# Kernel tuning notes

Hardware: AMD Instinct MI355X
Metric: run time of the kernel (lower is better)

Reference implementation:

```python
import jax, jax.numpy as jnp
import numpy as np

B, M = 32768, 200
NUM_LAYERS, OW, OH = 22, 11, 11
CNN_CH, HIDDEN = 128, 512
ACTION_NVEC = (9, 10)


def setup_inputs() -> dict:
    key = jax.random.key(0)
    ks = jax.random.split(key, 16)
    s = 0.02
    inp = {
        "observations": jax.random.randint(ks[0], (B, M, 3), 0, 256, dtype=jnp.int32),
        "max_vec": jnp.ones((NUM_LAYERS,), dtype=jnp.float32),
        "w_conv1": jax.random.normal(ks[1], (CNN_CH, NUM_LAYERS, 5, 5), jnp.float32) * s,
        "b_conv1": jnp.zeros((CNN_CH,), jnp.float32),
        "w_conv2": jax.random.normal(ks[2], (CNN_CH, CNN_CH, 3, 3), jnp.float32) * s,
        "b_conv2": jnp.zeros((CNN_CH,), jnp.float32),
        "w_fc": jax.random.normal(ks[3], (CNN_CH, HIDDEN // 2), jnp.float32) * s,
        "b_fc": jnp.zeros((HIDDEN // 2,), jnp.float32),
        "w_self": jax.random.normal(ks[4], (NUM_LAYERS, HIDDEN // 2), jnp.float32) * s,
        "b_self": jnp.zeros((HIDDEN // 2,), jnp.float32),
        "w_actor0": jax.random.normal(ks[5], (HIDDEN, ACTION_NVEC[0]), jnp.float32) * 0.01,
        "b_actor0": jnp.zeros((ACTION_NVEC[0],), jnp.float32),
        "w_actor1": jax.random.normal(ks[6], (HIDDEN, ACTION_NVEC[1]), jnp.float32) * 0.01,
        "b_actor1": jnp.zeros((ACTION_NVEC[1],), jnp.float32),
        "w_value": jax.random.normal(ks[7], (HIDDEN, 1), jnp.float32) * s,
        "b_value": jnp.zeros((1,), jnp.float32),
    }
    return inp


def _conv(x, w, b, stride):
    y = jax.lax.conv_general_dilated(
        x, w, window_strides=(stride, stride), padding="VALID",
        dimension_numbers=("NCHW", "OIHW", "NCHW"))
    return y + b[None, :, None, None]


def _encode(observations, max_vec, w_conv1, b_conv1, w_conv2, b_conv2,
            w_fc, b_fc, w_self, b_self):
    # torch: token_observations[token_observations == 255] = 0
    obs = jnp.where(observations == 255, 0, observations)
    coords = obs[..., 0]                       # [B, M]
    x_idx = (coords >> 4) & 15
    y_idx = coords & 15
    atr_idx = obs[..., 1]
    atr_val = obs[..., 2].astype(jnp.float32)
    # coords_byte != 255 is always True after the 255->0 rewrite above
    valid = (x_idx < OW) & (y_idx < OH) & (atr_idx < NUM_LAYERS)
    b_idx = jnp.broadcast_to(jnp.arange(obs.shape[0])[:, None], coords.shape)
    # route invalid tokens to a dummy batch slot B, then drop it
    b_idx = jnp.where(valid, b_idx, obs.shape[0])
    a_idx = jnp.where(valid, atr_idx, 0)
    xs = jnp.where(valid, x_idx, 0)
    ys = jnp.where(valid, y_idx, 0)
    box = jnp.zeros((obs.shape[0] + 1, NUM_LAYERS, OW, OH), jnp.float32)
    box = box.at[b_idx, a_idx, xs, ys].set(atr_val)[: obs.shape[0]]
    features = box / max_vec[None, :, None, None]
    self_feat = jax.nn.relu(features[:, :, 5, 5] @ w_self + b_self)   # [B, 256]
    h = jax.nn.relu(_conv(features, w_conv1, b_conv1, 3))             # [B,128,3,3]
    h = jax.nn.relu(_conv(h, w_conv2, b_conv2, 1))                    # [B,128,1,1]
    h = h.reshape(h.shape[0], -1)                                     # [B,128]
    cnn_feat = jax.nn.relu(h @ w_fc + b_fc)                           # [B,256]
    return jnp.concatenate([self_feat, cnn_feat], axis=1)             # [B,512]


def reference(observations, max_vec, w_conv1, b_conv1, w_conv2, b_conv2,
              w_fc, b_fc, w_self, b_self, w_actor0, b_actor0,
              w_actor1, b_actor1, w_value, b_value):
    hidden = _encode(observations, max_vec, w_conv1, b_conv1, w_conv2, b_conv2,
                     w_fc, b_fc, w_self, b_self)
    logits0 = hidden @ w_actor0 + b_actor0
    logits1 = hidden @ w_actor1 + b_actor1
    value = hidden @ w_value + b_value
    return (logits0, logits1, value, hidden)
```

## Files before the change

kernel.cpp:

```cpp
#include <hip/hip_runtime.h>
#include <hip/hip_bf16.h>

typedef unsigned int uint;
typedef unsigned short ushort;
typedef unsigned long long ull;
typedef __attribute__((ext_vector_type(8))) short short8;
typedef __attribute__((ext_vector_type(4))) float float4_;

#define B_TOT 32768
#define NL    22
#define HID0  ((long)B_TOT * 20)

#define W2F_OFF  0
#define WFCF_OFF 294912
#define WHF_OFF  360448
#define W1T_OFF  393216
#define H1_OFF   674816

__device__ __forceinline__ ushort f2bf(float v) {
  uint x = __float_as_uint(v);
  x += 0x7fffu + ((x >> 16) & 1u);
  return (ushort)(x >> 16);
}

__device__ __forceinline__ uint cvtpk(float lo, float hi) {
  uint r;
  asm volatile("v_cvt_pk_bf16_f32 %0, %1, %2" : "=v"(r) : "v"(lo), "v"(hi));
  return r;
}

extern "C" __global__ __launch_bounds__(256)
void k_prep(const float* __restrict__ wc1, const float* __restrict__ wc2,
            const float* __restrict__ wfc,
            const float* __restrict__ wa0, const float* __restrict__ wa1,
            const float* __restrict__ wv,
            ushort* __restrict__ w2f, ushort* __restrict__ wfcf,
            ushort* __restrict__ whf, float* __restrict__ w1t)
{
  int i = blockIdx.x * 256 + threadIdx.x;
  if (i < 18432) {
    int l = i & 63, cg = (i >> 6) & 7, ks = i >> 9;
    int col = cg * 16 + (l & 15), kb = ks * 32 + (l >> 4) * 8;
    ushort t[8];
    #pragma unroll
    for (int j = 0; j < 8; ++j) t[j] = f2bf(wc2[col * 1152 + kb + j]);
    uint4 o = { (uint)t[0]|((uint)t[1]<<16), (uint)t[2]|((uint)t[3]<<16),
                (uint)t[4]|((uint)t[5]<<16), (uint)t[6]|((uint)t[7]<<16) };
    ((uint4*)w2f)[i] = o;
  } else if (i < 22528) {
    int i2 = i - 18432;
    int l = i2 & 63, cg = (i2 >> 6) & 15, ks = i2 >> 10;
    int col = cg * 16 + (l & 15), kb = ks * 32 + (l >> 4) * 8;
    ushort t[8];
    #pragma unroll
    for (int j = 0; j < 8; ++j) t[j] = f2bf(wfc[(kb + j) * 256 + col]);
    uint4 o = { (uint)t[0]|((uint)t[1]<<16), (uint)t[2]|((uint)t[3]<<16),
                (uint)t[4]|((uint)t[5]<<16), (uint)t[6]|((uint)t[7]<<16) };
    ((uint4*)wfcf)[i2] = o;
  } else if (i < 24576) {
    int i2 = i - 22528;
    int l = i2 & 63, cg = (i2 >> 6) & 1, ks = i2 >> 7;
    int col = cg * 16 + (l & 15), kb = ks * 32 + (l >> 4) * 8;
    ushort t[8];
    #pragma unroll
    for (int j = 0; j < 8; ++j) {
      int k = kb + j;
      float v = (col < 9)  ? wa0[k*9 + col]
              : (col < 19) ? wa1[k*10 + (col - 9)]
              : (col == 19) ? wv[k] : 0.f;
      t[j] = f2bf(v);
    }
    uint4 o = { (uint)t[0]|((uint)t[1]<<16), (uint)t[2]|((uint)t[3]<<16),
                (uint)t[4]|((uint)t[5]<<16), (uint)t[6]|((uint)t[7]<<16) };
    ((uint4*)whf)[i2] = o;
  } else if (i < 24576 + 70400) {
    int j = i - 24576;
    int oc = j & 127, r = j >> 7;
    w1t[j] = wc1[oc * 550 + r];
  }
}

extern "C" __global__ __launch_bounds__(256)
void k_encode(const int* __restrict__ obs, const float* __restrict__ maxvec,
              const float* __restrict__ w1t, const float* __restrict__ bc1,
              const float* __restrict__ wself, const float* __restrict__ bself,
              float* __restrict__ out, ushort* __restrict__ h1g)
{
  __shared__ uint klist[4][64];

  const int tid = threadIdx.x, lane = tid & 63, w = tid >> 6;
  const long b = (long)blockIdx.x * 4 + w;

  float rm_own = (lane < NL) ? (1.0f / maxvec[lane]) : 0.f;

  const uint* ob = (const uint*)obs + b * 600;
  int cnt = 0;
  #pragma unroll
  for (int r = 0; r < 4; ++r) {
    int m = r * 64 + lane;
    bool valid = false; uint pk = 0;
    if (m < 200) {
      uint c = ob[m*3], a = ob[m*3+1], v = ob[m*3+2];
      c = (c == 255u) ? 0u : c;  a = (a == 255u) ? 0u : a;  v = (v == 255u) ? 0u : v;
      uint x = (c >> 4) & 15u, y = c & 15u;
      valid = (x < 11u) && (y < 11u) && (a < NL);
      pk = (a << 16) | (x << 12) | (y << 8) | v;
    }
    ull bal = __ballot(valid);
    if (valid) {
      int pos = cnt + __popcll(bal & ((1ull << lane) - 1ull));
      if (pos < 64) klist[w][pos] = pk;
    }
    cnt += __popcll(bal);
  }
  if (cnt > 64) cnt = 64;

  uint u = (lane < cnt) ? klist[w][lane] : 0xffffffffu;
  uint cell = u >> 8;
  bool alive = (lane < cnt);
  for (int d = 1; d < cnt; ++d) {
    uint oc_ = __shfl_down(cell, d);
    alive = alive && !((lane + d < cnt) && (oc_ == cell));
  }
  ull bal2 = __ballot(alive);
  const int n2 = __popcll(bal2);
  if (alive) klist[w][__popcll(bal2 & ((1ull << lane) - 1ull))] = u;

  float a0[9] = {0,0,0,0,0,0,0,0,0}, a1[9] = {0,0,0,0,0,0,0,0,0};
  float2 sa = {0.f, 0.f}, sb = {0.f, 0.f};
  uint tk = klist[w][0];
  for (int t = 0; t < n2; ++t) {
    uint cur = tk;
    tk = klist[w][(t + 1) & 63];
    int a = cur >> 16, x = (cur >> 12) & 15, y = (cur >> 8) & 15;
    float fv = (float)(cur & 255u) * __shfl(rm_own, a);
    if (x == 5 && y == 5) {
      const float2* ws2 = (const float2*)(wself + a * 256);
      float2 w0 = ws2[lane], w1 = ws2[64 + lane];
      sa.x = fmaf(fv, w0.x, sa.x);  sa.y = fmaf(fv, w0.y, sa.y);
      sb.x = fmaf(fv, w1.x, sb.x);  sb.y = fmaf(fv, w1.y, sb.y);
    }
    #pragma unroll
    for (int ox = 0; ox < 3; ++ox) {
      int kx = x - 3 * ox;
      if ((unsigned)kx > 4u) continue;
      #pragma unroll
      for (int oy = 0; oy < 3; ++oy) {
        int ky = y - 3 * oy;
        if ((unsigned)ky > 4u) continue;
        float2 wv2 = ((const float2*)(w1t + (a*25 + kx*5 + ky) * 128))[lane];
        a0[ox*3+oy] = fmaf(fv, wv2.x, a0[ox*3+oy]);
        a1[ox*3+oy] = fmaf(fv, wv2.y, a1[ox*3+oy]);
      }
    }
  }

  {
    const float2* bs2 = (const float2*)bself;
    float2 b0_ = bs2[lane], b1_ = bs2[64 + lane];
    float2 o0 = { fmaxf(sa.x + b0_.x, 0.f), fmaxf(sa.y + b0_.y, 0.f) };
    float2 o1 = { fmaxf(sb.x + b1_.x, 0.f), fmaxf(sb.y + b1_.y, 0.f) };
    float2* out2 = (float2*)(out + HID0 + b * 512);
    out2[lane] = o0;
    out2[64 + lane] = o1;
  }

  {
    const float2 bc = ((const float2*)bc1)[lane];
    float v0[9], v1[9];
    #pragma unroll
    for (int p = 0; p < 9; ++p) {
      v0[p] = fmaxf(a0[p] + bc.x, 0.f);
      v1[p] = fmaxf(a1[p] + bc.y, 0.f);
    }
    uint wds[9];
    wds[0] = cvtpk(v0[0], v0[1]);
    wds[1] = cvtpk(v0[2], v0[3]);
    wds[2] = cvtpk(v0[4], v0[5]);
    wds[3] = cvtpk(v0[6], v0[7]);
    wds[4] = cvtpk(v0[8], v1[0]);
    wds[5] = cvtpk(v1[1], v1[2]);
    wds[6] = cvtpk(v1[3], v1[4]);
    wds[7] = cvtpk(v1[5], v1[6]);
    wds[8] = cvtpk(v1[7], v1[8]);
    uint* dst = (uint*)h1g + b * 576 + 9 * lane;
    #pragma unroll
    for (int j = 0; j < 9; ++j) dst[j] = wds[j];
  }
}

extern "C" __global__ __launch_bounds__(256)
void k_mlp(const ushort* __restrict__ h1g, const ushort* __restrict__ w2f,
           const float* __restrict__ bc2, const ushort* __restrict__ wfcf,
           const float* __restrict__ bfc, const ushort* __restrict__ whf,
           const float* __restrict__ ba0, const float* __restrict__ ba1,
           const float* __restrict__ bv, float* __restrict__ out)
{
  __shared__ short  Abuf[2][4][64][8];
  __shared__ ushort h2A[16][64][8];

  const int tid = threadIdx.x, lane = tid & 63, w = tid >> 6;
  const int lo = lane & 15, hi = lane >> 4;
  const int bb = blockIdx.x, b0 = bb * 64;

  const short8* w2fv  = (const short8*)w2f;
  const short8* wfcfv = (const short8*)wfcf;
  const uint4*  A4    = (const uint4*)h1g;
  const long    arow  = (long)(b0 + (tid >> 2)) * 144 + (tid & 3);

  float4_ acc[4][2];
  #pragma unroll
  for (int cgi = 0; cgi < 2; ++cgi) {
    float bv_ = bc2[(2*w + cgi)*16 + lo];
    float4_ t = {bv_, bv_, bv_, bv_};
    #pragma unroll
    for (int m = 0; m < 4; ++m) acc[m][cgi] = t;
  }

  uint4 rA = A4[arow];
  for (int t = 0; t < 36; ++t) {
    const int cur = t & 1;
    *(uint4*)&Abuf[cur][tid & 3][tid >> 2][0] = rA;
    if (t + 1 < 36) rA = A4[arow + (t + 1) * 4];
    __syncthreads();
    short8 af[4];
    #pragma unroll
    for (int m = 0; m < 4; ++m)
      af[m] = *(const short8*)&Abuf[cur][hi][m*16 + lo][0];
    #pragma unroll
    for (int cgi = 0; cgi < 2; ++cgi) {
      short8 bf = w2fv[(t*8 + 2*w + cgi)*64 + lane];
      #pragma unroll
      for (int m = 0; m < 4; ++m)
        acc[m][cgi] = __builtin_amdgcn_mfma_f32_16x16x32_bf16(af[m], bf, acc[m][cgi], 0, 0, 0);
    }
  }
  __syncthreads();

  #pragma unroll
  for (int cgi = 0; cgi < 2; ++cgi) {
    int col = (2*w + cgi)*16 + lo;
    #pragma unroll
    for (int m = 0; m < 4; ++m)
      #pragma unroll
      for (int q = 0; q < 4; ++q) {
        int R = m*16 + hi*4 + q;
        h2A[col >> 3][R][col & 7] = f2bf(fmaxf(acc[m][cgi][q], 0.f));
      }
  }
  __syncthreads();

  float4_ acc2[4][4];
  #pragma unroll
  for (int cgi = 0; cgi < 4; ++cgi) {
    float bv_ = bfc[(4*w + cgi)*16 + lo];
    float4_ t = {bv_, bv_, bv_, bv_};
    #pragma unroll
    for (int m = 0; m < 4; ++m) acc2[m][cgi] = t;
  }
  #pragma unroll
  for (int ks = 0; ks < 4; ++ks) {
    short8 af[4];
    #pragma unroll
    for (int m = 0; m < 4; ++m)
      af[m] = *(const short8*)&h2A[ks*4 + hi][m*16 + lo][0];
    #pragma unroll
    for (int cgi = 0; cgi < 4; ++cgi) {
      short8 bf = wfcfv[(ks*16 + 4*w + cgi)*64 + lane];
      #pragma unroll
      for (int m = 0; m < 4; ++m)
        acc2[m][cgi] = __builtin_amdgcn_mfma_f32_16x16x32_bf16(af[m], bf, acc2[m][cgi], 0, 0, 0);
    }
  }

  #pragma unroll
  for (int cgi = 0; cgi < 4; ++cgi) {
    int col = (4*w + cgi)*16 + lo;
    #pragma unroll
    for (int m = 0; m < 4; ++m)
      #pragma unroll
      for (int q = 0; q < 4; ++q) {
        int R = m*16 + hi*4 + q;
        out[HID0 + (long)(b0 + R)*512 + 256 + col] = fmaxf(acc2[m][cgi][q], 0.f);
      }
  }
  __syncthreads();

  const short8* whfv = (const short8*)whf;
  float4_ acc3[2];
  #pragma unroll
  for (int cg = 0; cg < 2; ++cg) {
    int col = cg*16 + lo;
    float bias = (col < 9) ? ba0[col] : (col < 19) ? ba1[col - 9]
               : (col == 19) ? bv[0] : 0.f;
    float4_ t = {bias, bias, bias, bias};
    acc3[cg] = t;
  }

  const float* hrow = out + HID0 + (long)(b0 + w*16 + lo) * 512;
  #pragma unroll
  for (int ks = 0; ks < 16; ++ks) {
    float4_ f0 = *(const float4_*)(hrow + ks*32 + hi*8);
    float4_ f1 = *(const float4_*)(hrow + ks*32 + hi*8 + 4);
    union { short8 s; ushort u[8]; } afu;
    afu.u[0] = f2bf(f0[0]); afu.u[1] = f2bf(f0[1]);
    afu.u[2] = f2bf(f0[2]); afu.u[3] = f2bf(f0[3]);
    afu.u[4] = f2bf(f1[0]); afu.u[5] = f2bf(f1[1]);
    afu.u[6] = f2bf(f1[2]); afu.u[7] = f2bf(f1[3]);
    #pragma unroll
    for (int cg = 0; cg < 2; ++cg) {
      short8 bf = whfv[(ks*2 + cg)*64 + lane];
      acc3[cg] = __builtin_amdgcn_mfma_f32_16x16x32_bf16(afu.s, bf, acc3[cg], 0, 0, 0);
    }
  }

  #pragma unroll
  for (int cg = 0; cg < 2; ++cg) {
    int col = cg*16 + lo;
    #pragma unroll
    for (int q = 0; q < 4; ++q) {
      long R = b0 + w*16 + hi*4 + q;
      float v = acc3[cg][q];
      if (col < 9)        out[R*9 + col] = v;
      else if (col < 19)  out[(long)B_TOT*9 + R*10 + (col - 9)] = v;
      else if (col == 19) out[(long)B_TOT*19 + R] = v;
    }
  }
}

extern "C" void kernel_launch(void* const* d_in, const int* in_sizes, int n_in,
                              void* d_out, int out_size, void* d_ws, size_t ws_size,
                              hipStream_t stream) {
  const int* obs      = (const int*)d_in[0];
  const float* maxvec = (const float*)d_in[1];
  const float* wc1    = (const float*)d_in[2];
  const float* bc1    = (const float*)d_in[3];
  const float* wc2    = (const float*)d_in[4];
  const float* bc2    = (const float*)d_in[5];
  const float* wfc    = (const float*)d_in[6];
  const float* bfc    = (const float*)d_in[7];
  const float* wself  = (const float*)d_in[8];
  const float* bself  = (const float*)d_in[9];
  const float* wa0    = (const float*)d_in[10];
  const float* ba0    = (const float*)d_in[11];
  const float* wa1    = (const float*)d_in[12];
  const float* ba1    = (const float*)d_in[13];
  const float* wv     = (const float*)d_in[14];
  const float* bv     = (const float*)d_in[15];
  float* out          = (float*)d_out;

  char* ws = (char*)d_ws;
  ushort* w2f  = (ushort*)(ws + W2F_OFF);
  ushort* wfcf = (ushort*)(ws + WFCF_OFF);
  ushort* whf  = (ushort*)(ws + WHF_OFF);
  float*  w1t  = (float*)(ws + W1T_OFF);
  ushort* h1g  = (ushort*)(ws + H1_OFF);

  k_prep  <<<dim3(371),      dim3(256), 0, stream>>>(wc1, wc2, wfc, wa0, wa1, wv,
                                                     w2f, wfcf, whf, w1t);
  k_encode<<<dim3(B_TOT/4),  dim3(256), 0, stream>>>(obs, maxvec, w1t, bc1,
                                                     wself, bself, out, h1g);
  k_mlp   <<<dim3(B_TOT/64), dim3(256), 0, stream>>>(h1g, w2f, bc2, wfcf, bfc,
                                                     whf, ba0, ba1, bv, out);
}
```

Baseline: 109.5 us.

## Fuse encoder and MLP kernels, keeping conv1 activations in LDS

Merges the token-scatter/conv1 encoder and the conv2/fc/head MLP into one kernel that processes 32 samples per block. The conv1 output stays in shared memory instead of going through a global workspace, and conv2 weights are re-laid out (channel-major within position) to match. Token broadcast now uses readfirstlane/readlane instead of shuffles. The cost is about 77KB of LDS per block, which lowers occupancy, each wave runs 8 samples serially, and the MFMA tiles shrink to 32 rows.

New measurement: 161.6 us. 1.48x slower.

```diff
diff --git a/kernel.cpp b/kernel.cpp
--- a/kernel.cpp
+++ b/kernel.cpp
@@ -15,14 +15,15 @@
 #define WFCF_OFF 294912
 #define WHF_OFF  360448
 #define W1T_OFF  393216
-#define H1_OFF   674816
+
+#define H1_LDS_BYTES 76032
+#define LDS_TOTAL    77056
 
 __device__ __forceinline__ ushort f2bf(float v) {
   uint x = __float_as_uint(v);
   x += 0x7fffu + ((x >> 16) & 1u);
   return (ushort)(x >> 16);
 }
-
 __device__ __forceinline__ uint cvtpk(float lo, float hi) {
   uint r;
   asm volatile("v_cvt_pk_bf16_f32 %0, %1, %2" : "=v"(r) : "v"(lo), "v"(hi));
@@ -43,7 +44,10 @@
     int col = cg * 16 + (l & 15), kb = ks * 32 + (l >> 4) * 8;
     ushort t[8];
     #pragma unroll
-    for (int j = 0; j < 8; ++j) t[j] = f2bf(wc2[col * 1152 + kb + j]);
+    for (int j = 0; j < 8; ++j) {
+      int kp = kb + j, ic = kp & 127, p = kp >> 7;
+      t[j] = f2bf(wc2[col * 1152 + ic * 9 + p]);
+    }
     uint4 o = { (uint)t[0]|((uint)t[1]<<16), (uint)t[2]|((uint)t[3]<<16),
                 (uint)t[4]|((uint)t[5]<<16), (uint)t[6]|((uint)t[7]<<16) };
     ((uint4*)w2f)[i] = o;
@@ -81,203 +85,175 @@
 }
 
 extern "C" __global__ __launch_bounds__(256)
-void k_encode(const int* __restrict__ obs, const float* __restrict__ maxvec,
-              const float* __restrict__ w1t, const float* __restrict__ bc1,
-              const float* __restrict__ wself, const float* __restrict__ bself,
-              float* __restrict__ out, ushort* __restrict__ h1g)
+void k_main(const int* __restrict__ obs, const float* __restrict__ maxvec,
+            const float* __restrict__ w1t, const float* __restrict__ bc1,
+            const float* __restrict__ wself, const float* __restrict__ bself,
+            const ushort* __restrict__ w2f, const float* __restrict__ bc2,
+            const ushort* __restrict__ wfcf, const float* __restrict__ bfc,
+            const ushort* __restrict__ whf,
+            const float* __restrict__ ba0, const float* __restrict__ ba1,
+            const float* __restrict__ bv, float* __restrict__ out)
 {
-  __shared__ uint klist[4][64];
-
-  const int tid = threadIdx.x, lane = tid & 63, w = tid >> 6;
-  const long b = (long)blockIdx.x * 4 + w;
-
-  float rm_own = (lane < NL) ? (1.0f / maxvec[lane]) : 0.f;
-
-  const uint* ob = (const uint*)obs + b * 600;
-  int cnt = 0;
-  #pragma unroll
-  for (int r = 0; r < 4; ++r) {
-    int m = r * 64 + lane;
-    bool valid = false; uint pk = 0;
-    if (m < 200) {
-      uint c = ob[m*3], a = ob[m*3+1], v = ob[m*3+2];
-      c = (c == 255u) ? 0u : c;  a = (a == 255u) ? 0u : a;  v = (v == 255u) ? 0u : v;
-      uint x = (c >> 4) & 15u, y = c & 15u;
-      valid = (x < 11u) && (y < 11u) && (a < NL);
-      pk = (a << 16) | (x << 12) | (y << 8) | v;
-    }
-    ull bal = __ballot(valid);
-    if (valid) {
-      int pos = cnt + __popcll(bal & ((1ull << lane) - 1ull));
-      if (pos < 64) klist[w][pos] = pk;
-    }
-    cnt += __popcll(bal);
-  }
-  if (cnt > 64) cnt = 64;
-
-  uint u = (lane < cnt) ? klist[w][lane] : 0xffffffffu;
-  uint cell = u >> 8;
-  bool alive = (lane < cnt);
-  for (int d = 1; d < cnt; ++d) {
-    uint oc_ = __shfl_down(cell, d);
-    alive = alive && !((lane + d < cnt) && (oc_ == cell));
-  }
-  ull bal2 = __ballot(alive);
-  const int n2 = __popcll(bal2);
-  if (alive) klist[w][__popcll(bal2 & ((1ull << lane) - 1ull))] = u;
-
-  float a0[9] = {0,0,0,0,0,0,0,0,0}, a1[9] = {0,0,0,0,0,0,0,0,0};
-  float2 sa = {0.f, 0.f}, sb = {0.f, 0.f};
-  uint tk = klist[w][0];
-  for (int t = 0; t < n2; ++t) {
-    uint cur = tk;
-    tk = klist[w][(t + 1) & 63];
-    int a = cur >> 16, x = (cur >> 12) & 15, y = (cur >> 8) & 15;
-    float fv = (float)(cur & 255u) * __shfl(rm_own, a);
-    if (x == 5 && y == 5) {
-      const float2* ws2 = (const float2*)(wself + a * 256);
-      float2 w0 = ws2[lane], w1 = ws2[64 + lane];
-      sa.x = fmaf(fv, w0.x, sa.x);  sa.y = fmaf(fv, w0.y, sa.y);
-      sb.x = fmaf(fv, w1.x, sb.x);  sb.y = fmaf(fv, w1.y, sb.y);
-    }
-    #pragma unroll
-    for (int ox = 0; ox < 3; ++ox) {
-      int kx = x - 3 * ox;
-      if ((unsigned)kx > 4u) continue;
-      #pragma unroll
-      for (int oy = 0; oy < 3; ++oy) {
-        int ky = y - 3 * oy;
-        if ((unsigned)ky > 4u) continue;
-        float2 wv2 = ((const float2*)(w1t + (a*25 + kx*5 + ky) * 128))[lane];
-        a0[ox*3+oy] = fmaf(fv, wv2.x, a0[ox*3+oy]);
-        a1[ox*3+oy] = fmaf(fv, wv2.y, a1[ox*3+oy]);
-      }
-    }
-  }
-
-  {
-    const float2* bs2 = (const float2*)bself;
-    float2 b0_ = bs2[lane], b1_ = bs2[64 + lane];
-    float2 o0 = { fmaxf(sa.x + b0_.x, 0.f), fmaxf(sa.y + b0_.y, 0.f) };
-    float2 o1 = { fmaxf(sb.x + b1_.x, 0.f), fmaxf(sb.y + b1_.y, 0.f) };
-    float2* out2 = (float2*)(out + HID0 + b * 512);
-    out2[lane] = o0;
-    out2[64 + lane] = o1;
-  }
-
-  {
-    const float2 bc = ((const float2*)bc1)[lane];
-    float v0[9], v1[9];
-    #pragma unroll
-    for (int p = 0; p < 9; ++p) {
-      v0[p] = fmaxf(a0[p] + bc.x, 0.f);
-      v1[p] = fmaxf(a1[p] + bc.y, 0.f);
-    }
-    uint wds[9];
-    wds[0] = cvtpk(v0[0], v0[1]);
-    wds[1] = cvtpk(v0[2], v0[3]);
-    wds[2] = cvtpk(v0[4], v0[5]);
-    wds[3] = cvtpk(v0[6], v0[7]);
-    wds[4] = cvtpk(v0[8], v1[0]);
-    wds[5] = cvtpk(v1[1], v1[2]);
-    wds[6] = cvtpk(v1[3], v1[4]);
-    wds[7] = cvtpk(v1[5], v1[6]);
-    wds[8] = cvtpk(v1[7], v1[8]);
-    uint* dst = (uint*)h1g + b * 576 + 9 * lane;
-    #pragma unroll
-    for (int j = 0; j < 9; ++j) dst[j] = wds[j];
-  }
-}
-
-extern "C" __global__ __launch_bounds__(256)
-void k_mlp(const ushort* __restrict__ h1g, const ushort* __restrict__ w2f,
-           const float* __restrict__ bc2, const ushort* __restrict__ wfcf,
-           const float* __restrict__ bfc, const ushort* __restrict__ whf,
-           const float* __restrict__ ba0, const float* __restrict__ ba1,
-           const float* __restrict__ bv, float* __restrict__ out)
-{
-  __shared__ short  Abuf[2][4][64][8];
-  __shared__ ushort h2A[16][64][8];
+  extern __shared__ char smem[];
+  uint* h1w   = (uint*)smem;
+  uint* klist = (uint*)(smem + H1_LDS_BYTES);
 
   const int tid = threadIdx.x, lane = tid & 63, w = tid >> 6;
   const int lo = lane & 15, hi = lane >> 4;
-  const int bb = blockIdx.x, b0 = bb * 64;
-
-  const short8* w2fv  = (const short8*)w2f;
-  const short8* wfcfv = (const short8*)wfcf;
-  const uint4*  A4    = (const uint4*)h1g;
-  const long    arow  = (long)(b0 + (tid >> 2)) * 144 + (tid & 3);
-
-  float4_ acc[4][2];
+  const int b0 = blockIdx.x * 32;
+
+  float rm_own = (lane < NL) ? (1.0f / maxvec[lane]) : 0.f;
+  const float2 bcp  = ((const float2*)bc1)[lane];
+  const float2 bsp0 = ((const float2*)bself)[lane];
+  const float2 bsp1 = ((const float2*)bself)[64 + lane];
+  uint* kl = klist + w * 64;
+
+  for (int s = 0; s < 8; ++s) {
+    const int  r = w * 8 + s;
+    const long b = b0 + r;
+    const uint* ob = (const uint*)obs + b * 600;
+
+    int cnt = 0;
+    #pragma unroll
+    for (int rr = 0; rr < 4; ++rr) {
+      int m = rr * 64 + lane;
+      bool valid = false; uint pk = 0;
+      if (m < 200) {
+        uint c = ob[m*3], a = ob[m*3+1], v = ob[m*3+2];
+        c = (c == 255u) ? 0u : c;  a = (a == 255u) ? 0u : a;  v = (v == 255u) ? 0u : v;
+        uint x = (c >> 4) & 15u, y = c & 15u;
+        valid = (x < 11u) && (y < 11u) && (a < NL);
+        pk = (a << 16) | (x << 12) | (y << 8) | v;
+      }
+      ull bal = __ballot(valid);
+      if (valid) {
+        int pos = cnt + __popcll(bal & ((1ull << lane) - 1ull));
+        if (pos < 64) kl[pos] = pk;
+      }
+      cnt += __popcll(bal);
+    }
+    if (cnt > 64) cnt = 64;
+
+    uint u = (lane < cnt) ? kl[lane] : 0xffffffffu;
+    uint cell = u >> 8;
+    bool alive = (lane < cnt);
+    for (int d = 1; d < cnt; ++d) {
+      uint oc_ = __shfl_down(cell, d);
+      alive = alive && !((lane + d < cnt) && (oc_ == cell));
+    }
+    ull bal2 = __ballot(alive);
+    const int n2 = __popcll(bal2);
+    if (alive) kl[__popcll(bal2 & ((1ull << lane) - 1ull))] = u;
+
+    float a0[9] = {0,0,0,0,0,0,0,0,0}, a1[9] = {0,0,0,0,0,0,0,0,0};
+    float2 sa = {0.f,0.f}, sb = {0.f,0.f};
+    uint nxt = kl[0];
+    for (int t = 0; t < n2; ++t) {
+      uint curv = nxt;
+      nxt = kl[(t + 1) & 63];
+      uint cur = (uint)__builtin_amdgcn_readfirstlane((int)curv);
+      int a = cur >> 16, x = (cur >> 12) & 15, y = (cur >> 8) & 15;
+      float rmv = __int_as_float(
+          __builtin_amdgcn_readlane(__float_as_int(rm_own), a));
+      float fv = (float)(cur & 255u) * rmv;
+      if (x == 5 && y == 5) {
+        const float2* ws2 = (const float2*)(wself + a * 256);
+        float2 w0 = ws2[lane], w1 = ws2[64 + lane];
+        sa.x = fmaf(fv, w0.x, sa.x);  sa.y = fmaf(fv, w0.y, sa.y);
+        sb.x = fmaf(fv, w1.x, sb.x);  sb.y = fmaf(fv, w1.y, sb.y);
+      }
+      #pragma unroll
+      for (int ox = 0; ox < 3; ++ox) {
+        int kx = x - 3 * ox;
+        if ((unsigned)kx > 4u) continue;
+        #pragma unroll
+        for (int oy = 0; oy < 3; ++oy) {
+          int ky = y - 3 * oy;
+          if ((unsigned)ky > 4u) continue;
+          int widx = a * 25 + kx * 5 + ky;
+          float2 wv2 = ((const float2*)w1t)[widx * 64 + lane];
+          a0[ox*3+oy] = fmaf(fv, wv2.x, a0[ox*3+oy]);
+          a1[ox*3+oy] = fmaf(fv, wv2.y, a1[ox*3+oy]);
+        }
+      }
+    }
+
+    {
+      float2 o0 = { fmaxf(sa.x + bsp0.x, 0.f), fmaxf(sa.y + bsp0.y, 0.f) };
+      float2 o1 = { fmaxf(sb.x + bsp1.x, 0.f), fmaxf(sb.y + bsp1.y, 0.f) };
+      float2* out2 = (float2*)(out + HID0 + b * 512);
+      out2[lane] = o0;
+      out2[64 + lane] = o1;
+    }
+
+    #pragma unroll
+    for (int p = 0; p < 9; ++p) {
+      uint val = cvtpk(fmaxf(a0[p] + bcp.x, 0.f), fmaxf(a1[p] + bcp.y, 0.f));
+      h1w[(p * 16 + (lane >> 2)) * 132 + r * 4 + (lane & 3)] = val;
+    }
+  }
+  __syncthreads();
+
+  const short8* w2fv = (const short8*)w2f;
+  float4_ acc[2][2];
   #pragma unroll
   for (int cgi = 0; cgi < 2; ++cgi) {
     float bv_ = bc2[(2*w + cgi)*16 + lo];
     float4_ t = {bv_, bv_, bv_, bv_};
-    #pragma unroll
-    for (int m = 0; m < 4; ++m) acc[m][cgi] = t;
-  }
-
-  uint4 rA = A4[arow];
+    acc[0][cgi] = t; acc[1][cgi] = t;
+  }
   for (int t = 0; t < 36; ++t) {
-    const int cur = t & 1;
-    *(uint4*)&Abuf[cur][tid & 3][tid >> 2][0] = rA;
-    if (t + 1 < 36) rA = A4[arow + (t + 1) * 4];
-    __syncthreads();
-    short8 af[4];
-    #pragma unroll
-    for (int m = 0; m < 4; ++m)
-      af[m] = *(const short8*)&Abuf[cur][hi][m*16 + lo][0];
+    const char* ap = smem + (size_t)(t*4 + hi) * 528;
+    short8 af0 = *(const short8*)(ap + lo * 16);
+    short8 af1 = *(const short8*)(ap + (16 + lo) * 16);
     #pragma unroll
     for (int cgi = 0; cgi < 2; ++cgi) {
       short8 bf = w2fv[(t*8 + 2*w + cgi)*64 + lane];
-      #pragma unroll
-      for (int m = 0; m < 4; ++m)
-        acc[m][cgi] = __builtin_amdgcn_mfma_f32_16x16x32_bf16(af[m], bf, acc[m][cgi], 0, 0, 0);
+      acc[0][cgi] = __builtin_amdgcn_mfma_f32_16x16x32_bf16(af0, bf, acc[0][cgi], 0, 0, 0);
+      acc[1][cgi] = __builtin_amdgcn_mfma_f32_16x16x32_bf16(af1, bf, acc[1][cgi], 0, 0, 0);
     }
   }
   __syncthreads();
 
+  ushort* h2A = (ushort*)smem;
   #pragma unroll
   for (int cgi = 0; cgi < 2; ++cgi) {
     int col = (2*w + cgi)*16 + lo;
     #pragma unroll
-    for (int m = 0; m < 4; ++m)
+    for (int m = 0; m < 2; ++m)
       #pragma unroll
       for (int q = 0; q < 4; ++q) {
         int R = m*16 + hi*4 + q;
-        h2A[col >> 3][R][col & 7] = f2bf(fmaxf(acc[m][cgi][q], 0.f));
+        h2A[((col >> 3) * 32 + R) * 8 + (col & 7)] =
+            f2bf(fmaxf(acc[m][cgi][q], 0.f));
       }
   }
   __syncthreads();
 
-  float4_ acc2[4][4];
+  float4_ acc2[2][4];
   #pragma unroll
   for (int cgi = 0; cgi < 4; ++cgi) {
     float bv_ = bfc[(4*w + cgi)*16 + lo];
     float4_ t = {bv_, bv_, bv_, bv_};
-    #pragma unroll
-    for (int m = 0; m < 4; ++m) acc2[m][cgi] = t;
-  }
+    acc2[0][cgi] = t; acc2[1][cgi] = t;
+  }
+  const short8* wfcfv = (const short8*)wfcf;
   #pragma unroll
   for (int ks = 0; ks < 4; ++ks) {
-    short8 af[4];
-    #pragma unroll
-    for (int m = 0; m < 4; ++m)
-      af[m] = *(const short8*)&h2A[ks*4 + hi][m*16 + lo][0];
+    short8 af0 = *(const short8*)&h2A[((ks*4 + hi) * 32 + lo) * 8];
+    short8 af1 = *(const short8*)&h2A[((ks*4 + hi) * 32 + 16 + lo) * 8];
     #pragma unroll
     for (int cgi = 0; cgi < 4; ++cgi) {
       short8 bf = wfcfv[(ks*16 + 4*w + cgi)*64 + lane];
-      #pragma unroll
-      for (int m = 0; m < 4; ++m)
-        acc2[m][cgi] = __builtin_amdgcn_mfma_f32_16x16x32_bf16(af[m], bf, acc2[m][cgi], 0, 0, 0);
-    }
-  }
-
+      acc2[0][cgi] = __builtin_amdgcn_mfma_f32_16x16x32_bf16(af0, bf, acc2[0][cgi], 0, 0, 0);
+      acc2[1][cgi] = __builtin_amdgcn_mfma_f32_16x16x32_bf16(af1, bf, acc2[1][cgi], 0, 0, 0);
+    }
+  }
   #pragma unroll
   for (int cgi = 0; cgi < 4; ++cgi) {
     int col = (4*w + cgi)*16 + lo;
     #pragma unroll
-    for (int m = 0; m < 4; ++m)
+    for (int m = 0; m < 2; ++m)
       #pragma unroll
       for (int q = 0; q < 4; ++q) {
         int R = m*16 + hi*4 + q;
@@ -287,17 +263,16 @@
   __syncthreads();
 
   const short8* whfv = (const short8*)whf;
-  float4_ acc3[2];
-  #pragma unroll
-  for (int cg = 0; cg < 2; ++cg) {
-    int col = cg*16 + lo;
+  const int hm = w >> 1, hcg = w & 1;
+  float4_ acc3;
+  {
+    int col = hcg*16 + lo;
     float bias = (col < 9) ? ba0[col] : (col < 19) ? ba1[col - 9]
                : (col == 19) ? bv[0] : 0.f;
     float4_ t = {bias, bias, bias, bias};
-    acc3[cg] = t;
-  }
-
-  const float* hrow = out + HID0 + (long)(b0 + w*16 + lo) * 512;
+    acc3 = t;
+  }
+  const float* hrow = out + HID0 + (long)(b0 + hm*16 + lo) * 512;
   #pragma unroll
   for (int ks = 0; ks < 16; ++ks) {
     float4_ f0 = *(const float4_*)(hrow + ks*32 + hi*8);
@@ -307,20 +282,15 @@
     afu.u[2] = f2bf(f0[2]); afu.u[3] = f2bf(f0[3]);
     afu.u[4] = f2bf(f1[0]); afu.u[5] = f2bf(f1[1]);
     afu.u[6] = f2bf(f1[2]); afu.u[7] = f2bf(f1[3]);
-    #pragma unroll
-    for (int cg = 0; cg < 2; ++cg) {
-      short8 bf = whfv[(ks*2 + cg)*64 + lane];
-      acc3[cg] = __builtin_amdgcn_mfma_f32_16x16x32_bf16(afu.s, bf, acc3[cg], 0, 0, 0);
-    }
-  }
-
-  #pragma unroll
-  for (int cg = 0; cg < 2; ++cg) {
-    int col = cg*16 + lo;
+    short8 bf = whfv[(ks*2 + hcg)*64 + lane];
+    acc3 = __builtin_amdgcn_mfma_f32_16x16x32_bf16(afu.s, bf, acc3, 0, 0, 0);
+  }
+  {
+    int col = hcg*16 + lo;
     #pragma unroll
     for (int q = 0; q < 4; ++q) {
-      long R = b0 + w*16 + hi*4 + q;
-      float v = acc3[cg][q];
+      long R = b0 + hm*16 + hi*4 + q;
+      float v = acc3[q];
       if (col < 9)        out[R*9 + col] = v;
       else if (col < 19)  out[(long)B_TOT*9 + R*10 + (col - 9)] = v;
       else if (col == 19) out[(long)B_TOT*19 + R] = v;
@@ -354,12 +324,13 @@
   ushort* wfcf = (ushort*)(ws + WFCF_OFF);
   ushort* whf  = (ushort*)(ws + WHF_OFF);
   float*  w1t  = (float*)(ws + W1T_OFF);
-  ushort* h1g  = (ushort*)(ws + H1_OFF);
-
-  k_prep  <<<dim3(371),      dim3(256), 0, stream>>>(wc1, wc2, wfc, wa0, wa1, wv,
-                                                     w2f, wfcf, whf, w1t);
-  k_encode<<<dim3(B_TOT/4),  dim3(256), 0, stream>>>(obs, maxvec, w1t, bc1,
-                                                     wself, bself, out, h1g);
-  k_mlp   <<<dim3(B_TOT/64), dim3(256), 0, stream>>>(h1g, w2f, bc2, wfcf, bfc,
-                                                     whf, ba0, ba1, bv, out);
-}
+
+  hipFuncSetAttribute((const void*)k_main,
+                      hipFuncAttributeMaxDynamicSharedMemorySize, LDS_TOTAL);
+
+  k_prep<<<dim3(371),       dim3(256), 0, stream>>>(wc1, wc2, wfc, wa0, wa1, wv,
+                                                    w2f, wfcf, whf, w1t);
+  k_main<<<dim3(B_TOT/32),  dim3(256), LDS_TOTAL, stream>>>(
+      obs, maxvec, w1t, bc1, wself, bself, w2f, bc2, wfcf, bfc,
+      whf, ba0, ba1, bv, out);
+}
```

## Store conv1 weights as packed bf16 and make token loop branch-free with scalar broadcasts

Applied to the files above, without the earlier changes.

Conv1 weights are now converted to bf16 and packed two output channels per 32-bit word, which halves the weight table and the per-lane loads in the scatter-accumulate loop. The token fields and the per-layer scale are read with readfirstlane/readlane so they live in scalar registers instead of going through a shuffle. The 3x3 window loop no longer branches: it always loads a weight and zeroes the contribution when the tap is out of range. The cost is lower weight precision and extra loads for the masked taps.

New measurement: 118.9 us. +8.5%, slower.

```diff
diff --git a/kernel.cpp b/kernel.cpp
--- a/kernel.cpp
+++ b/kernel.cpp
@@ -14,15 +14,14 @@
 #define W2F_OFF  0
 #define WFCF_OFF 294912
 #define WHF_OFF  360448
-#define W1T_OFF  393216
-#define H1_OFF   674816
+#define W1P_OFF  393216
+#define H1_OFF   534016
 
 __device__ __forceinline__ ushort f2bf(float v) {
   uint x = __float_as_uint(v);
   x += 0x7fffu + ((x >> 16) & 1u);
   return (ushort)(x >> 16);
 }
-
 __device__ __forceinline__ uint cvtpk(float lo, float hi) {
   uint r;
   asm volatile("v_cvt_pk_bf16_f32 %0, %1, %2" : "=v"(r) : "v"(lo), "v"(hi));
@@ -35,7 +34,7 @@
             const float* __restrict__ wa0, const float* __restrict__ wa1,
             const float* __restrict__ wv,
             ushort* __restrict__ w2f, ushort* __restrict__ wfcf,
-            ushort* __restrict__ whf, float* __restrict__ w1t)
+            ushort* __restrict__ whf, uint* __restrict__ w1p)
 {
   int i = blockIdx.x * 256 + threadIdx.x;
   if (i < 18432) {
@@ -73,16 +72,18 @@
     uint4 o = { (uint)t[0]|((uint)t[1]<<16), (uint)t[2]|((uint)t[3]<<16),
                 (uint)t[4]|((uint)t[5]<<16), (uint)t[6]|((uint)t[7]<<16) };
     ((uint4*)whf)[i2] = o;
-  } else if (i < 24576 + 70400) {
+  } else if (i < 24576 + 35200) {
     int j = i - 24576;
-    int oc = j & 127, r = j >> 7;
-    w1t[j] = wc1[oc * 550 + r];
+    int l = j & 63, r = j >> 6;
+    ushort lo_ = f2bf(wc1[(2*l)     * 550 + r]);
+    ushort hi_ = f2bf(wc1[(2*l + 1) * 550 + r]);
+    w1p[j] = (uint)lo_ | ((uint)hi_ << 16);
   }
 }
 
 extern "C" __global__ __launch_bounds__(256)
 void k_encode(const int* __restrict__ obs, const float* __restrict__ maxvec,
-              const float* __restrict__ w1t, const float* __restrict__ bc1,
+              const uint* __restrict__ w1p, const float* __restrict__ bc1,
               const float* __restrict__ wself, const float* __restrict__ bself,
               float* __restrict__ out, ushort* __restrict__ h1g)
 {
@@ -127,30 +128,37 @@
   if (alive) klist[w][__popcll(bal2 & ((1ull << lane) - 1ull))] = u;
 
   float a0[9] = {0,0,0,0,0,0,0,0,0}, a1[9] = {0,0,0,0,0,0,0,0,0};
-  float2 sa = {0.f, 0.f}, sb = {0.f, 0.f};
-  uint tk = klist[w][0];
+  float2 sa = {0.f,0.f}, sb = {0.f,0.f};
+  uint nxt = klist[w][0];
   for (int t = 0; t < n2; ++t) {
-    uint cur = tk;
-    tk = klist[w][(t + 1) & 63];
+    uint curv = nxt;
+    nxt = klist[w][(t + 1) & 63];
+    uint cur = (uint)__builtin_amdgcn_readfirstlane((int)curv);
     int a = cur >> 16, x = (cur >> 12) & 15, y = (cur >> 8) & 15;
-    float fv = (float)(cur & 255u) * __shfl(rm_own, a);
+    float rmv = __int_as_float(
+        __builtin_amdgcn_readlane(__float_as_int(rm_own), a));
+    float fv = (float)(cur & 255u) * rmv;
     if (x == 5 && y == 5) {
       const float2* ws2 = (const float2*)(wself + a * 256);
       float2 w0 = ws2[lane], w1 = ws2[64 + lane];
       sa.x = fmaf(fv, w0.x, sa.x);  sa.y = fmaf(fv, w0.y, sa.y);
       sb.x = fmaf(fv, w1.x, sb.x);  sb.y = fmaf(fv, w1.y, sb.y);
     }
+    const int wbase = a * 25;
     #pragma unroll
     for (int ox = 0; ox < 3; ++ox) {
       int kx = x - 3 * ox;
-      if ((unsigned)kx > 4u) continue;
       #pragma unroll
       for (int oy = 0; oy < 3; ++oy) {
         int ky = y - 3 * oy;
-        if ((unsigned)ky > 4u) continue;
-        float2 wv2 = ((const float2*)(w1t + (a*25 + kx*5 + ky) * 128))[lane];
-        a0[ox*3+oy] = fmaf(fv, wv2.x, a0[ox*3+oy]);
-        a1[ox*3+oy] = fmaf(fv, wv2.y, a1[ox*3+oy]);
+        bool ok = ((unsigned)kx <= 4u) & ((unsigned)ky <= 4u);
+        int widx = ok ? (wbase + kx * 5 + ky) : 0;
+        uint wu = w1p[widx * 64 + lane];
+        float fvp = ok ? fv : 0.f;
+        float wx = __uint_as_float(wu << 16);
+        float wy = __uint_as_float(wu & 0xffff0000u);
+        a0[ox*3+oy] = fmaf(fvp, wx, a0[ox*3+oy]);
+        a1[ox*3+oy] = fmaf(fvp, wy, a1[ox*3+oy]);
       }
     }
   }
@@ -353,12 +361,12 @@
   ushort* w2f  = (ushort*)(ws + W2F_OFF);
   ushort* wfcf = (ushort*)(ws + WFCF_OFF);
   ushort* whf  = (ushort*)(ws + WHF_OFF);
-  float*  w1t  = (float*)(ws + W1T_OFF);
+  uint*   w1p  = (uint*)(ws + W1P_OFF);
   ushort* h1g  = (ushort*)(ws + H1_OFF);
 
-  k_prep  <<<dim3(371),      dim3(256), 0, stream>>>(wc1, wc2, wfc, wa0, wa1, wv,
-                                                     w2f, wfcf, whf, w1t);
-  k_encode<<<dim3(B_TOT/4),  dim3(256), 0, stream>>>(obs, maxvec, w1t, bc1,
+  k_prep  <<<dim3(234),      dim3(256), 0, stream>>>(wc1, wc2, wfc, wa0, wa1, wv,
+                                                     w2f, wfcf, whf, w1p);
+  k_encode<<<dim3(B_TOT/4),  dim3(256), 0, stream>>>(obs, maxvec, w1p, bc1,
                                                      wself, bself, out, h1g);
   k_mlp   <<<dim3(B_TOT/64), dim3(256), 0, stream>>>(h1g, w2f, bc2, wfcf, bfc,
                                                      whf, ba0, ba1, bv, out);
```
